# Kernel tuning notes

Measured on AMD Instinct MI355X. Metric: run time of the kernel, lower is better.

Reference implementation:

```python
import jax, jax.numpy as jnp
import numpy as np

N, D, E, C = 50000, 128, 500000, 2
K1, K2 = 3, 5


def spline_conv(x, src, dst, pseudo, W, root, bias, K, num_nodes):
    # degree-1 open B-spline basis over dim=1 pseudo coords in [0,1]
    v = pseudo[:, 0] * (K - 1)                      # [E]
    i0f = jnp.floor(v)
    frac = v - i0f                                   # [E]
    i0 = jnp.clip(i0f.astype(jnp.int32), 0, K - 1)
    i1 = jnp.clip(i0 + 1, 0, K - 1)
    xs = x[src]                                      # [E, D] gather
    # scatter basis-weighted neighbor feats into per-(node,kernel) buckets
    acc = jax.ops.segment_sum((1.0 - frac)[:, None] * xs, dst * K + i0,
                              num_segments=num_nodes * K)
    acc = acc + jax.ops.segment_sum(frac[:, None] * xs, dst * K + i1,
                                    num_segments=num_nodes * K)
    acc = acc.reshape(num_nodes, K, -1)              # [N, K, D]
    deg = jax.ops.segment_sum(jnp.ones_like(v), dst, num_segments=num_nodes)
    out = jnp.einsum('nkd,kdo->no', acc, W) / jnp.maximum(deg, 1.0)[:, None]
    return out + x @ root + bias                     # mean aggr + root + bias


def setup_inputs() -> dict:
    key = jax.random.key(0)
    ks = jax.random.split(key, 12)
    s = 1.0 / np.sqrt(D)
    return {
        'x': jax.random.normal(ks[0], (N, D), jnp.float32),
        'edge_index': jax.random.randint(ks[1], (2, E), 0, N, jnp.int64),
        'edge_attr': jax.random.uniform(ks[2], (E, 1), jnp.float32),
        'W1': jax.random.normal(ks[3], (K1, D, D), jnp.float32) * s,
        'root1': jax.random.normal(ks[4], (D, D), jnp.float32) * s,
        'b1': jnp.zeros((D,), jnp.float32),
        'W2': jax.random.normal(ks[5], (K2, D, D), jnp.float32) * s,
        'root2': jax.random.normal(ks[6], (D, D), jnp.float32) * s,
        'b2': jnp.zeros((D,), jnp.float32),
        'Wm': jax.random.normal(ks[7], (D, C), jnp.float32) * s,
        'bm': jnp.zeros((C,), jnp.float32),
    }


def reference(x, edge_index, edge_attr, W1, root1, b1, W2, root2, b2, Wm, bm):
    src, dst = edge_index[0], edge_index[1]
    h = jax.nn.elu(spline_conv(x, src, dst, edge_attr, W1, root1, b1, K1, N))
    # dropout is identity in eval mode
    h = jax.nn.elu(spline_conv(h, src, dst, edge_attr, W2, root2, b2, K2, N))
    return jax.nn.relu(h @ Wm + bm)                  # [N, C]
```

## Files before the change

kernel.cpp:

```cpp
#include <hip/hip_runtime.h>
#include <cmath>


typedef __attribute__((ext_vector_type(8))) short bf16x8;
typedef __attribute__((ext_vector_type(4))) float f32x4;

static inline int cdiv(int a, int b) { return (a + b - 1) / b; }

__device__ __forceinline__ float bf2f(unsigned short u) {
  unsigned v = ((unsigned)u) << 16;
  return __builtin_bit_cast(float, v);
}
__device__ __forceinline__ unsigned short f2bf(float f) {
  unsigned u = __builtin_bit_cast(unsigned, f);
  u += 0x7FFFu + ((u >> 16) & 1u);
  return (unsigned short)(u >> 16);
}
__device__ __forceinline__ float elu1(float v) {
  return v > 0.f ? v : (expf(v) - 1.f);
}

__global__ void hist_kernel(const int* __restrict__ ei, int E,
                            int* __restrict__ cnt) {
  int e = blockIdx.x * blockDim.x + threadIdx.x;
  if (e < E) atomicAdd(&cnt[ei[E + e]], 1);
}

__global__ void scan_partials_kernel(const int* __restrict__ cnt, int N,
                                     int* __restrict__ partials) {
  __shared__ int red[256];
  int base = blockIdx.x * 1024;
  int s = 0;
  for (int i = threadIdx.x; i < 1024; i += 256) {
    int idx = base + i;
    if (idx < N) s += cnt[idx];
  }
  red[threadIdx.x] = s;
  __syncthreads();
  for (int off = 128; off > 0; off >>= 1) {
    if (threadIdx.x < off) red[threadIdx.x] += red[threadIdx.x + off];
    __syncthreads();
  }
  if (threadIdx.x == 0) partials[blockIdx.x] = red[0];
}

__global__ void scan_pscan_kernel(const int* __restrict__ partials, int nb,
                                  int* __restrict__ pscan) {
  __shared__ int tmp[256];
  int t = threadIdx.x;
  int v = (t < nb) ? partials[t] : 0;
  tmp[t] = v;
  __syncthreads();
  for (int off = 1; off < 256; off <<= 1) {
    int u = (t >= off) ? tmp[t - off] : 0;
    __syncthreads();
    tmp[t] += u;
    __syncthreads();
  }
  pscan[t + 1] = tmp[t];
  if (t == 0) pscan[0] = 0;
}

__global__ void scan_apply_kernel(const int* __restrict__ cnt, int N,
                                  const int* __restrict__ pscan, int nb,
                                  int* __restrict__ rowptr, int* __restrict__ cursor) {
  __shared__ int tsum[256];
  int t = threadIdx.x;
  int base = blockIdx.x * 1024 + t * 4;
  int v0 = 0, v1 = 0, v2 = 0, v3 = 0;
  if (base + 0 < N) v0 = cnt[base + 0];
  if (base + 1 < N) v1 = cnt[base + 1];
  if (base + 2 < N) v2 = cnt[base + 2];
  if (base + 3 < N) v3 = cnt[base + 3];
  int s = v0 + v1 + v2 + v3;
  tsum[t] = s;
  __syncthreads();
  for (int off = 1; off < 256; off <<= 1) {
    int u = (t >= off) ? tsum[t - off] : 0;
    __syncthreads();
    tsum[t] += u;
    __syncthreads();
  }
  int excl = pscan[blockIdx.x] + tsum[t] - s;
  if (base + 0 < N) { rowptr[base + 0] = excl; cursor[base + 0] = excl; excl += v0; }
  if (base + 1 < N) { rowptr[base + 1] = excl; cursor[base + 1] = excl; excl += v1; }
  if (base + 2 < N) { rowptr[base + 2] = excl; cursor[base + 2] = excl; excl += v2; }
  if (base + 3 < N) { rowptr[base + 3] = excl; cursor[base + 3] = excl; excl += v3; }
  if (blockIdx.x == 0 && t == 0) rowptr[N] = pscan[nb];
}

__global__ void scatter_kernel(const int* __restrict__ ei,
                               const float* __restrict__ ea, int E,
                               int* __restrict__ cursor, int2* __restrict__ es) {
  int e = blockIdx.x * blockDim.x + threadIdx.x;
  if (e < E) {
    int dst = ei[E + e];
    int pos = atomicAdd(&cursor[dst], 1);
    es[pos] = make_int2(ei[e], __float_as_int(ea[e]));
  }
}

__global__ void cvt_x_kernel(const float* __restrict__ x,
                             unsigned short* __restrict__ xb, int n4) {
  for (int i = blockIdx.x * blockDim.x + threadIdx.x; i < n4;
       i += gridDim.x * blockDim.x) {
    float4 v = ((const float4*)x)[i];
    ushort4 o;
    o.x = f2bf(v.x); o.y = f2bf(v.y); o.z = f2bf(v.z); o.w = f2bf(v.w);
    ((ushort4*)xb)[i] = o;
  }
}

__global__ void build_btf_kernel(const float* __restrict__ W,
                                 const float* __restrict__ root,
                                 unsigned short* __restrict__ BtF, int KD, int KT) {
  int idx = blockIdx.x * blockDim.x + threadIdx.x;
  if (idx >= 128 * KT) return;
  int G = idx >> 9;
  int r = idx & 511;
  int lane = r >> 3;
  int j = r & 7;
  int ks = G >> 3;
  int ni = G & 7;
  int col = ni * 16 + (lane & 15);
  int k = ks * 32 + (lane >> 4) * 8 + j;
  float v = (k < KD) ? W[(size_t)k * 128 + col] : root[(size_t)(k - KD) * 128 + col];
  BtF[idx] = f2bf(v);
}

template <int K, int KT, bool FINAL>
__global__ __launch_bounds__(256, 4) void fused_layer(
    const unsigned short* __restrict__ Xc,
    const int* __restrict__ rowptr, const int2* __restrict__ es,
    const unsigned short* __restrict__ BtF,
    const float* __restrict__ bias,
    unsigned short* __restrict__ Hout,
    const float* __restrict__ Wm, const float* __restrict__ bm,
    float* __restrict__ FOut) {
  constexpr int LDK = KT + 8;
  constexpr int NKS = KT / 32;
  __shared__ unsigned short Asub[16][LDK];
  __shared__ float hred[4][16][2];

  const int w = threadIdx.x >> 6;
  const int lane = threadIdx.x & 63;
  const int lr = lane & 15;
  const int kg = lane >> 4;
  const int node0 = blockIdx.x * 16;

  for (int i = 0; i < 4; ++i) {
    const int r = w * 4 + i;
    const int node = node0 + r;
    float accx[K], accy[K];
#pragma unroll
    for (int k = 0; k < K; ++k) { accx[k] = 0.f; accy[k] = 0.f; }
    const int beg = rowptr[node], end = rowptr[node + 1];
    int e = beg;
    for (; e + 8 <= end; e += 8) {
      int2 sp[8];
#pragma unroll
      for (int t = 0; t < 8; ++t) sp[t] = es[e + t];
      ushort2 xv[8];
#pragma unroll
      for (int t = 0; t < 8; ++t)
        xv[t] = *(const ushort2*)(Xc + (size_t)sp[t].x * 128 + 2 * lane);
#pragma unroll
      for (int t = 0; t < 8; ++t) {
        float v = __int_as_float(sp[t].y) * (float)(K - 1);
        int i0 = min((int)v, K - 2);
        float fr = v - (float)i0;
        float w0 = 1.f - fr;
        float xx = bf2f(xv[t].x), xy = bf2f(xv[t].y);
        int i0u = __builtin_amdgcn_readfirstlane(i0);
#pragma unroll
        for (int k = 0; k < K - 1; ++k) {
          if (i0u == k) {
            accx[k] = fmaf(w0, xx, accx[k]);
            accy[k] = fmaf(w0, xy, accy[k]);
            accx[k + 1] = fmaf(fr, xx, accx[k + 1]);
            accy[k + 1] = fmaf(fr, xy, accy[k + 1]);
          }
        }
      }
    }
    for (; e < end; e += 4) {
      const int last = end - 1;
      int2 sp[4];
      bool okv[4];
#pragma unroll
      for (int t = 0; t < 4; ++t) {
        okv[t] = (e + t <= last);
        sp[t] = es[okv[t] ? (e + t) : last];
      }
      ushort2 xv[4];
#pragma unroll
      for (int t = 0; t < 4; ++t)
        xv[t] = *(const ushort2*)(Xc + (size_t)sp[t].x * 128 + 2 * lane);
#pragma unroll
      for (int t = 0; t < 4; ++t) {
        float v = __int_as_float(sp[t].y) * (float)(K - 1);
        int i0 = min((int)v, K - 2);
        float fr = v - (float)i0;
        float w0 = 1.f - fr;
        if (!okv[t]) { w0 = 0.f; fr = 0.f; }
        float xx = bf2f(xv[t].x), xy = bf2f(xv[t].y);
        int i0u = __builtin_amdgcn_readfirstlane(i0);
#pragma unroll
        for (int k = 0; k < K - 1; ++k) {
          if (i0u == k) {
            accx[k] = fmaf(w0, xx, accx[k]);
            accy[k] = fmaf(w0, xy, accy[k]);
            accx[k + 1] = fmaf(fr, xx, accx[k + 1]);
            accy[k + 1] = fmaf(fr, xy, accy[k + 1]);
          }
        }
      }
    }
    float deg = (float)(end - beg);
    float sc = 1.f / fmaxf(deg, 1.f);
#pragma unroll
    for (int k = 0; k < K; ++k) {
      ushort2 o;
      o.x = f2bf(accx[k] * sc);
      o.y = f2bf(accy[k] * sc);
      *(ushort2*)&Asub[r][k * 128 + 2 * lane] = o;
    }
    ushort2 own = *(const ushort2*)(Xc + (size_t)node * 128 + 2 * lane);
    *(ushort2*)&Asub[r][K * 128 + 2 * lane] = own;
  }
  __syncthreads();

  const int ni0 = w * 2;
  f32x4 acc[2];
  acc[0] = {0.f, 0.f, 0.f, 0.f};
  acc[1] = {0.f, 0.f, 0.f, 0.f};
#pragma unroll
  for (int ks = 0; ks < NKS; ++ks) {
    bf16x8 a = *(const bf16x8*)&Asub[lr][ks * 32 + kg * 8];
#pragma unroll
    for (int j = 0; j < 2; ++j) {
      bf16x8 b = *(const bf16x8*)(BtF + (size_t)(ks * 8 + ni0 + j) * 512 + lane * 8);
      acc[j] = __builtin_amdgcn_mfma_f32_16x16x32_bf16(a, b, acc[j], 0, 0, 0);
    }
  }

  float bv[2];
#pragma unroll
  for (int j = 0; j < 2; ++j) bv[j] = bias[(ni0 + j) * 16 + lr];

  if constexpr (!FINAL) {
#pragma unroll
    for (int r = 0; r < 4; ++r) {
      int row = kg * 4 + r;
      int node = node0 + row;
#pragma unroll
      for (int j = 0; j < 2; ++j) {
        float h = elu1(acc[j][r] + bv[j]);
        Hout[(size_t)node * 128 + (ni0 + j) * 16 + lr] = f2bf(h);
      }
    }
  } else {
    float wm0[2], wm1[2];
#pragma unroll
    for (int j = 0; j < 2; ++j) {
      float2 wv = *(const float2*)&Wm[((ni0 + j) * 16 + lr) * 2];
      wm0[j] = wv.x; wm1[j] = wv.y;
    }
#pragma unroll
    for (int r = 0; r < 4; ++r) {
      int row = kg * 4 + r;
      float t0 = 0.f, t1 = 0.f;
#pragma unroll
      for (int j = 0; j < 2; ++j) {
        float h = elu1(acc[j][r] + bv[j]);
        t0 = fmaf(h, wm0[j], t0);
        t1 = fmaf(h, wm1[j], t1);
      }
#pragma unroll
      for (int off = 8; off > 0; off >>= 1) {
        t0 += __shfl_down(t0, off);
        t1 += __shfl_down(t1, off);
      }
      if (lr == 0) {
        hred[w][row][0] = t0;
        hred[w][row][1] = t1;
      }
    }
    __syncthreads();
    if (threadIdx.x < 32) {
      int row = threadIdx.x >> 1;
      int c = threadIdx.x & 1;
      float s = hred[0][row][c] + hred[1][row][c] + hred[2][row][c] +
                hred[3][row][c] + bm[c];
      FOut[(size_t)(node0 + row) * 2 + c] = fmaxf(s, 0.f);
    }
  }
}

extern "C" void kernel_launch(void* const* d_in, const int* in_sizes, int n_in,
                              void* d_out, int out_size, void* d_ws, size_t ws_size,
                              hipStream_t stream) {
  const float* x = (const float*)d_in[0];
  const int* ei = (const int*)d_in[1];
  const float* ea = (const float*)d_in[2];
  const float* W1 = (const float*)d_in[3];
  const float* root1 = (const float*)d_in[4];
  const float* b1 = (const float*)d_in[5];
  const float* W2 = (const float*)d_in[6];
  const float* root2 = (const float*)d_in[7];
  const float* b2 = (const float*)d_in[8];
  const float* Wm = (const float*)d_in[9];
  const float* bm = (const float*)d_in[10];
  const int N = in_sizes[0] / 128;
  const int E = in_sizes[2];
  const int KT1 = 512, KT2 = 768;
  const int nb = cdiv(N, 1024);

  char* base = (char*)d_ws;
  size_t off = 0;
  auto alloc = [&](size_t bytes) -> void* {
    void* p = base + off;
    off += (bytes + 255) & ~(size_t)255;
    return p;
  };
  int* cnt = (int*)alloc((size_t)N * 4);
  int* rowptr = (int*)alloc((size_t)(N + 1) * 4);
  int* cursor = (int*)alloc((size_t)N * 4);
  int* partials = (int*)alloc(256 * 4);
  int* pscan = (int*)alloc(257 * 4);
  int2* es = (int2*)alloc((size_t)E * 8);
  unsigned short* xb = (unsigned short*)alloc((size_t)N * 128 * 2);
  unsigned short* h1 = (unsigned short*)alloc((size_t)N * 128 * 2);
  unsigned short* BtF1 = (unsigned short*)alloc((size_t)128 * KT1 * 2);
  unsigned short* BtF2 = (unsigned short*)alloc((size_t)128 * KT2 * 2);
  (void)ws_size; (void)n_in; (void)out_size;

  hipMemsetAsync(cnt, 0, (size_t)N * 4, stream);
  hist_kernel<<<cdiv(E, 256), 256, 0, stream>>>(ei, E, cnt);
  scan_partials_kernel<<<nb, 256, 0, stream>>>(cnt, N, partials);
  scan_pscan_kernel<<<1, 256, 0, stream>>>(partials, nb, pscan);
  scan_apply_kernel<<<nb, 256, 0, stream>>>(cnt, N, pscan, nb, rowptr, cursor);
  scatter_kernel<<<cdiv(E, 256), 256, 0, stream>>>(ei, ea, E, cursor, es);

  build_btf_kernel<<<cdiv(128 * KT1, 256), 256, 0, stream>>>(W1, root1, BtF1, 384, KT1);
  build_btf_kernel<<<cdiv(128 * KT2, 256), 256, 0, stream>>>(W2, root2, BtF2, 640, KT2);

  cvt_x_kernel<<<2048, 256, 0, stream>>>(x, xb, N * 32);

  const int nblk = N / 16;
  fused_layer<3, 512, false><<<nblk, 256, 0, stream>>>(
      xb, rowptr, es, BtF1, b1, h1, nullptr, nullptr, nullptr);
  fused_layer<5, 768, true><<<nblk, 256, 0, stream>>>(
      h1, rowptr, es, BtF2, b2, nullptr, Wm, bm, (float*)d_out);
}
```

Measured before the change: 189.3 us.

## Widen fused layer blocks to 32 nodes and gather edges in chunks of 16

```diff
diff --git a/kernel.cpp b/kernel.cpp
--- a/kernel.cpp
+++ b/kernel.cpp
@@ -128,94 +128,82 @@
   BtF[idx] = f2bf(v);
 }
 
+template <int K, bool MASK>
+__device__ __forceinline__ void agg_chunk16(
+    const unsigned short* __restrict__ Xc, const int2* __restrict__ es,
+    int e, int end, int lane, float (&accx)[K], float (&accy)[K]) {
+  const int last = end - 1;
+  int sx[16];
+  float pv[16];
+#pragma unroll
+  for (int t = 0; t < 16; ++t) {
+    int idx = MASK ? min(e + t, last) : (e + t);
+    int2 sp = es[idx];
+    sx[t] = sp.x;
+    pv[t] = __int_as_float(sp.y);
+  }
+  unsigned int dv[16];
+#pragma unroll
+  for (int t = 0; t < 16; ++t)
+    dv[t] = *(const unsigned int*)(Xc + (size_t)sx[t] * 128 + 2 * lane);
+#pragma unroll
+  for (int t = 0; t < 16; ++t) {
+    float v = pv[t] * (float)(K - 1);
+    int i0 = min((int)v, K - 2);
+    float fr = v - (float)i0;
+    float w0 = 1.f - fr;
+    if (MASK) {
+      bool ok = (e + t <= last);
+      fr = ok ? fr : 0.f;
+      w0 = ok ? w0 : 0.f;
+    }
+    float xx = __builtin_bit_cast(float, dv[t] << 16);
+    float xy = __builtin_bit_cast(float, dv[t] & 0xffff0000u);
+    int i0u = __builtin_amdgcn_readfirstlane(i0);
+#pragma unroll
+    for (int k = 0; k < K - 1; ++k) {
+      if (i0u == k) {
+        accx[k] = fmaf(w0, xx, accx[k]);
+        accy[k] = fmaf(w0, xy, accy[k]);
+        accx[k + 1] = fmaf(fr, xx, accx[k + 1]);
+        accy[k + 1] = fmaf(fr, xy, accy[k + 1]);
+      }
+    }
+  }
+}
+
 template <int K, int KT, bool FINAL>
-__global__ __launch_bounds__(256, 4) void fused_layer(
+__global__ __launch_bounds__(512, 6) void fused_layer(
     const unsigned short* __restrict__ Xc,
     const int* __restrict__ rowptr, const int2* __restrict__ es,
     const unsigned short* __restrict__ BtF,
     const float* __restrict__ bias,
     unsigned short* __restrict__ Hout,
     const float* __restrict__ Wm, const float* __restrict__ bm,
-    float* __restrict__ FOut) {
+    float* __restrict__ FOut, int N) {
   constexpr int LDK = KT + 8;
   constexpr int NKS = KT / 32;
-  __shared__ unsigned short Asub[16][LDK];
-  __shared__ float hred[4][16][2];
+  __shared__ unsigned short Asub[32][LDK];
+  __shared__ float hred[8][32][2];
 
   const int w = threadIdx.x >> 6;
   const int lane = threadIdx.x & 63;
   const int lr = lane & 15;
   const int kg = lane >> 4;
-  const int node0 = blockIdx.x * 16;
+  const int node0 = blockIdx.x * 32;
 
   for (int i = 0; i < 4; ++i) {
     const int r = w * 4 + i;
-    const int node = node0 + r;
+    const int node = min(node0 + r, N - 1);
     float accx[K], accy[K];
 #pragma unroll
     for (int k = 0; k < K; ++k) { accx[k] = 0.f; accy[k] = 0.f; }
     const int beg = rowptr[node], end = rowptr[node + 1];
     int e = beg;
-    for (; e + 8 <= end; e += 8) {
-      int2 sp[8];
-#pragma unroll
-      for (int t = 0; t < 8; ++t) sp[t] = es[e + t];
-      ushort2 xv[8];
-#pragma unroll
-      for (int t = 0; t < 8; ++t)
-        xv[t] = *(const ushort2*)(Xc + (size_t)sp[t].x * 128 + 2 * lane);
-#pragma unroll
-      for (int t = 0; t < 8; ++t) {
-        float v = __int_as_float(sp[t].y) * (float)(K - 1);
-        int i0 = min((int)v, K - 2);
-        float fr = v - (float)i0;
-        float w0 = 1.f - fr;
-        float xx = bf2f(xv[t].x), xy = bf2f(xv[t].y);
-        int i0u = __builtin_amdgcn_readfirstlane(i0);
-#pragma unroll
-        for (int k = 0; k < K - 1; ++k) {
-          if (i0u == k) {
-            accx[k] = fmaf(w0, xx, accx[k]);
-            accy[k] = fmaf(w0, xy, accy[k]);
-            accx[k + 1] = fmaf(fr, xx, accx[k + 1]);
-            accy[k + 1] = fmaf(fr, xy, accy[k + 1]);
-          }
-        }
-      }
-    }
-    for (; e < end; e += 4) {
-      const int last = end - 1;
-      int2 sp[4];
-      bool okv[4];
-#pragma unroll
-      for (int t = 0; t < 4; ++t) {
-        okv[t] = (e + t <= last);
-        sp[t] = es[okv[t] ? (e + t) : last];
-      }
-      ushort2 xv[4];
-#pragma unroll
-      for (int t = 0; t < 4; ++t)
-        xv[t] = *(const ushort2*)(Xc + (size_t)sp[t].x * 128 + 2 * lane);
-#pragma unroll
-      for (int t = 0; t < 4; ++t) {
-        float v = __int_as_float(sp[t].y) * (float)(K - 1);
-        int i0 = min((int)v, K - 2);
-        float fr = v - (float)i0;
-        float w0 = 1.f - fr;
-        if (!okv[t]) { w0 = 0.f; fr = 0.f; }
-        float xx = bf2f(xv[t].x), xy = bf2f(xv[t].y);
-        int i0u = __builtin_amdgcn_readfirstlane(i0);
-#pragma unroll
-        for (int k = 0; k < K - 1; ++k) {
-          if (i0u == k) {
-            accx[k] = fmaf(w0, xx, accx[k]);
-            accy[k] = fmaf(w0, xy, accy[k]);
-            accx[k + 1] = fmaf(fr, xx, accx[k + 1]);
-            accy[k + 1] = fmaf(fr, xy, accy[k + 1]);
-          }
-        }
-      }
-    }
+    for (; e + 16 <= end; e += 16)
+      agg_chunk16<K, false>(Xc, es, e, end, lane, accx, accy);
+    if (e < end)
+      agg_chunk16<K, true>(Xc, es, e, end, lane, accx, accy);
     float deg = (float)(end - beg);
     float sc = 1.f / fmaxf(deg, 1.f);
 #pragma unroll
@@ -230,69 +218,67 @@
   }
   __syncthreads();
 
-  const int ni0 = w * 2;
-  f32x4 acc[2];
-  acc[0] = {0.f, 0.f, 0.f, 0.f};
-  acc[1] = {0.f, 0.f, 0.f, 0.f};
+  const int ni = w;
+  f32x4 acc0 = {0.f, 0.f, 0.f, 0.f};
+  f32x4 acc1 = {0.f, 0.f, 0.f, 0.f};
+  __builtin_amdgcn_s_setprio(1);
 #pragma unroll
   for (int ks = 0; ks < NKS; ++ks) {
-    bf16x8 a = *(const bf16x8*)&Asub[lr][ks * 32 + kg * 8];
-#pragma unroll
-    for (int j = 0; j < 2; ++j) {
-      bf16x8 b = *(const bf16x8*)(BtF + (size_t)(ks * 8 + ni0 + j) * 512 + lane * 8);
-      acc[j] = __builtin_amdgcn_mfma_f32_16x16x32_bf16(a, b, acc[j], 0, 0, 0);
-    }
-  }
-
-  float bv[2];
-#pragma unroll
-  for (int j = 0; j < 2; ++j) bv[j] = bias[(ni0 + j) * 16 + lr];
+    bf16x8 b = *(const bf16x8*)(BtF + (size_t)(ks * 8 + ni) * 512 + lane * 8);
+    bf16x8 a0 = *(const bf16x8*)&Asub[lr][ks * 32 + kg * 8];
+    bf16x8 a1 = *(const bf16x8*)&Asub[16 + lr][ks * 32 + kg * 8];
+    acc0 = __builtin_amdgcn_mfma_f32_16x16x32_bf16(a0, b, acc0, 0, 0, 0);
+    acc1 = __builtin_amdgcn_mfma_f32_16x16x32_bf16(a1, b, acc1, 0, 0, 0);
+  }
+  __builtin_amdgcn_s_setprio(0);
+
+  const float bv = bias[ni * 16 + lr];
 
   if constexpr (!FINAL) {
 #pragma unroll
-    for (int r = 0; r < 4; ++r) {
-      int row = kg * 4 + r;
-      int node = node0 + row;
-#pragma unroll
-      for (int j = 0; j < 2; ++j) {
-        float h = elu1(acc[j][r] + bv[j]);
-        Hout[(size_t)node * 128 + (ni0 + j) * 16 + lr] = f2bf(h);
+    for (int mf = 0; mf < 2; ++mf) {
+      f32x4 a = mf ? acc1 : acc0;
+#pragma unroll
+      for (int r = 0; r < 4; ++r) {
+        int node = node0 + mf * 16 + kg * 4 + r;
+        if (node < N) {
+          float h = elu1(a[r] + bv);
+          Hout[(size_t)node * 128 + ni * 16 + lr] = f2bf(h);
+        }
       }
     }
   } else {
-    float wm0[2], wm1[2];
-#pragma unroll
-    for (int j = 0; j < 2; ++j) {
-      float2 wv = *(const float2*)&Wm[((ni0 + j) * 16 + lr) * 2];
-      wm0[j] = wv.x; wm1[j] = wv.y;
-    }
-#pragma unroll
-    for (int r = 0; r < 4; ++r) {
-      int row = kg * 4 + r;
-      float t0 = 0.f, t1 = 0.f;
-#pragma unroll
-      for (int j = 0; j < 2; ++j) {
-        float h = elu1(acc[j][r] + bv[j]);
-        t0 = fmaf(h, wm0[j], t0);
-        t1 = fmaf(h, wm1[j], t1);
+    float2 wv = *(const float2*)&Wm[(ni * 16 + lr) * 2];
+#pragma unroll
+    for (int mf = 0; mf < 2; ++mf) {
+      f32x4 a = mf ? acc1 : acc0;
+#pragma unroll
+      for (int r = 0; r < 4; ++r) {
+        float h = elu1(a[r] + bv);
+        float t0 = h * wv.x;
+        float t1 = h * wv.y;
+#pragma unroll
+        for (int off = 8; off > 0; off >>= 1) {
+          t0 += __shfl_down(t0, off);
+          t1 += __shfl_down(t1, off);
+        }
+        if (lr == 0) {
+          hred[w][mf * 16 + kg * 4 + r][0] = t0;
+          hred[w][mf * 16 + kg * 4 + r][1] = t1;
+        }
       }
-#pragma unroll
-      for (int off = 8; off > 0; off >>= 1) {
-        t0 += __shfl_down(t0, off);
-        t1 += __shfl_down(t1, off);
-      }
-      if (lr == 0) {
-        hred[w][row][0] = t0;
-        hred[w][row][1] = t1;
-      }
-    }
-    __syncthreads();
-    if (threadIdx.x < 32) {
+    }
+    __syncthreads();
+    if (threadIdx.x < 64) {
       int row = threadIdx.x >> 1;
       int c = threadIdx.x & 1;
-      float s = hred[0][row][c] + hred[1][row][c] + hred[2][row][c] +
-                hred[3][row][c] + bm[c];
-      FOut[(size_t)(node0 + row) * 2 + c] = fmaxf(s, 0.f);
+      int node = node0 + row;
+      if (node < N) {
+        float s = bm[c];
+#pragma unroll
+        for (int ww = 0; ww < 8; ++ww) s += hred[ww][row][c];
+        FOut[(size_t)node * 2 + c] = fmaxf(s, 0.f);
+      }
     }
   }
 }
@@ -347,9 +333,9 @@
 
   cvt_x_kernel<<<2048, 256, 0, stream>>>(x, xb, N * 32);
 
-  const int nblk = N / 16;
-  fused_layer<3, 512, false><<<nblk, 256, 0, stream>>>(
-      xb, rowptr, es, BtF1, b1, h1, nullptr, nullptr, nullptr);
-  fused_layer<5, 768, true><<<nblk, 256, 0, stream>>>(
-      h1, rowptr, es, BtF2, b2, nullptr, Wm, bm, (float*)d_out);
-}
+  const int nblk = cdiv(N, 32);
+  fused_layer<3, 512, false><<<nblk, 512, 0, stream>>>(
+      xb, rowptr, es, BtF1, b1, h1, nullptr, nullptr, nullptr, N);
+  fused_layer<5, 768, true><<<nblk, 512, 0, stream>>>(
+      h1, rowptr, es, BtF2, b2, nullptr, Wm, bm, (float*)d_out, N);
+}
```

After: 362.1 us. 91.3% more time.

## Process four nodes per wavefront with 16-byte row gathers and branchless spline weights

Applied to the files above, without the earlier changes.

```diff
diff --git a/kernel.cpp b/kernel.cpp
--- a/kernel.cpp
+++ b/kernel.cpp
@@ -148,99 +148,79 @@
   const int kg = lane >> 4;
   const int node0 = blockIdx.x * 16;
 
-  for (int i = 0; i < 4; ++i) {
-    const int r = w * 4 + i;
-    const int node = node0 + r;
-    float accx[K], accy[K];
-#pragma unroll
-    for (int k = 0; k < K; ++k) { accx[k] = 0.f; accy[k] = 0.f; }
-    const int beg = rowptr[node], end = rowptr[node + 1];
-    int e = beg;
-    for (; e + 8 <= end; e += 8) {
-      int2 sp[8];
-#pragma unroll
-      for (int t = 0; t < 8; ++t) sp[t] = es[e + t];
-      ushort2 xv[8];
-#pragma unroll
-      for (int t = 0; t < 8; ++t)
-        xv[t] = *(const ushort2*)(Xc + (size_t)sp[t].x * 128 + 2 * lane);
-#pragma unroll
-      for (int t = 0; t < 8; ++t) {
-        float v = __int_as_float(sp[t].y) * (float)(K - 1);
-        int i0 = min((int)v, K - 2);
-        float fr = v - (float)i0;
-        float w0 = 1.f - fr;
-        float xx = bf2f(xv[t].x), xy = bf2f(xv[t].y);
-        int i0u = __builtin_amdgcn_readfirstlane(i0);
-#pragma unroll
-        for (int k = 0; k < K - 1; ++k) {
-          if (i0u == k) {
-            accx[k] = fmaf(w0, xx, accx[k]);
-            accy[k] = fmaf(w0, xy, accy[k]);
-            accx[k + 1] = fmaf(fr, xx, accx[k + 1]);
-            accy[k + 1] = fmaf(fr, xy, accy[k + 1]);
-          }
-        }
-      }
-    }
-    for (; e < end; e += 4) {
-      const int last = end - 1;
-      int2 sp[4];
-      bool okv[4];
-#pragma unroll
-      for (int t = 0; t < 4; ++t) {
-        okv[t] = (e + t <= last);
-        sp[t] = es[okv[t] ? (e + t) : last];
-      }
-      ushort2 xv[4];
-#pragma unroll
-      for (int t = 0; t < 4; ++t)
-        xv[t] = *(const ushort2*)(Xc + (size_t)sp[t].x * 128 + 2 * lane);
-#pragma unroll
-      for (int t = 0; t < 4; ++t) {
-        float v = __int_as_float(sp[t].y) * (float)(K - 1);
-        int i0 = min((int)v, K - 2);
-        float fr = v - (float)i0;
-        float w0 = 1.f - fr;
-        if (!okv[t]) { w0 = 0.f; fr = 0.f; }
-        float xx = bf2f(xv[t].x), xy = bf2f(xv[t].y);
-        int i0u = __builtin_amdgcn_readfirstlane(i0);
-#pragma unroll
-        for (int k = 0; k < K - 1; ++k) {
-          if (i0u == k) {
-            accx[k] = fmaf(w0, xx, accx[k]);
-            accy[k] = fmaf(w0, xy, accy[k]);
-            accx[k + 1] = fmaf(fr, xx, accx[k + 1]);
-            accy[k + 1] = fmaf(fr, xy, accy[k + 1]);
-          }
-        }
-      }
-    }
-    float deg = (float)(end - beg);
-    float sc = 1.f / fmaxf(deg, 1.f);
-#pragma unroll
-    for (int k = 0; k < K; ++k) {
-      ushort2 o;
-      o.x = f2bf(accx[k] * sc);
-      o.y = f2bf(accy[k] * sc);
-      *(ushort2*)&Asub[r][k * 128 + 2 * lane] = o;
-    }
-    ushort2 own = *(const ushort2*)(Xc + (size_t)node * 128 + 2 * lane);
-    *(ushort2*)&Asub[r][K * 128 + 2 * lane] = own;
-  }
+  const int g = lane >> 4;
+  const int d16 = lane & 15;
+  const int r = w * 4 + g;
+  const int node = node0 + r;
+  const int beg = rowptr[node];
+  const int end = rowptr[node + 1];
+  const int deg = end - beg;
+
+  float acc[K][8];
+#pragma unroll
+  for (int k = 0; k < K; ++k)
+#pragma unroll
+    for (int j = 0; j < 8; ++j) acc[k][j] = 0.f;
+
+  const int mx = max(max(__shfl(deg, 0), __shfl(deg, 16)),
+                     max(__shfl(deg, 32), __shfl(deg, 48)));
+  const int lastc = max(end - 1, 0);
+
+  for (int s0 = 0; s0 < mx; s0 += 4) {
+    int2 sp[4];
+#pragma unroll
+    for (int t = 0; t < 4; ++t) sp[t] = es[min(beg + s0 + t, lastc)];
+    uint4 rv[4];
+#pragma unroll
+    for (int t = 0; t < 4; ++t)
+      rv[t] = *(const uint4*)(Xc + (size_t)sp[t].x * 128 + d16 * 8);
+#pragma unroll
+    for (int t = 0; t < 4; ++t) {
+      const bool ok = (s0 + t) < deg;
+      const float v = ok ? __int_as_float(sp[t].y) * (float)(K - 1) : -2.f;
+      float x[8];
+      x[0] = __builtin_bit_cast(float, rv[t].x << 16);
+      x[1] = __builtin_bit_cast(float, rv[t].x & 0xffff0000u);
+      x[2] = __builtin_bit_cast(float, rv[t].y << 16);
+      x[3] = __builtin_bit_cast(float, rv[t].y & 0xffff0000u);
+      x[4] = __builtin_bit_cast(float, rv[t].z << 16);
+      x[5] = __builtin_bit_cast(float, rv[t].z & 0xffff0000u);
+      x[6] = __builtin_bit_cast(float, rv[t].w << 16);
+      x[7] = __builtin_bit_cast(float, rv[t].w & 0xffff0000u);
+#pragma unroll
+      for (int k = 0; k < K; ++k) {
+        const float wk = fmaxf(1.f - fabsf(v - (float)k), 0.f);
+#pragma unroll
+        for (int j = 0; j < 8; ++j) acc[k][j] = fmaf(wk, x[j], acc[k][j]);
+      }
+    }
+  }
+
+  const float sc = 1.f / fmaxf((float)deg, 1.f);
+#pragma unroll
+  for (int k = 0; k < K; ++k) {
+    uint4 ov;
+    ov.x = (unsigned)f2bf(acc[k][0] * sc) | ((unsigned)f2bf(acc[k][1] * sc) << 16);
+    ov.y = (unsigned)f2bf(acc[k][2] * sc) | ((unsigned)f2bf(acc[k][3] * sc) << 16);
+    ov.z = (unsigned)f2bf(acc[k][4] * sc) | ((unsigned)f2bf(acc[k][5] * sc) << 16);
+    ov.w = (unsigned)f2bf(acc[k][6] * sc) | ((unsigned)f2bf(acc[k][7] * sc) << 16);
+    *(uint4*)&Asub[r][k * 128 + d16 * 8] = ov;
+  }
+  uint4 ownv = *(const uint4*)(Xc + (size_t)node * 128 + d16 * 8);
+  *(uint4*)&Asub[r][K * 128 + d16 * 8] = ownv;
   __syncthreads();
 
   const int ni0 = w * 2;
-  f32x4 acc[2];
-  acc[0] = {0.f, 0.f, 0.f, 0.f};
-  acc[1] = {0.f, 0.f, 0.f, 0.f};
+  f32x4 acc2[2];
+  acc2[0] = {0.f, 0.f, 0.f, 0.f};
+  acc2[1] = {0.f, 0.f, 0.f, 0.f};
 #pragma unroll
   for (int ks = 0; ks < NKS; ++ks) {
     bf16x8 a = *(const bf16x8*)&Asub[lr][ks * 32 + kg * 8];
 #pragma unroll
     for (int j = 0; j < 2; ++j) {
       bf16x8 b = *(const bf16x8*)(BtF + (size_t)(ks * 8 + ni0 + j) * 512 + lane * 8);
-      acc[j] = __builtin_amdgcn_mfma_f32_16x16x32_bf16(a, b, acc[j], 0, 0, 0);
+      acc2[j] = __builtin_amdgcn_mfma_f32_16x16x32_bf16(a, b, acc2[j], 0, 0, 0);
     }
   }
 
@@ -250,13 +230,13 @@
 
   if constexpr (!FINAL) {
 #pragma unroll
-    for (int r = 0; r < 4; ++r) {
-      int row = kg * 4 + r;
-      int node = node0 + row;
+    for (int rr = 0; rr < 4; ++rr) {
+      int row = kg * 4 + rr;
+      int onode = node0 + row;
 #pragma unroll
       for (int j = 0; j < 2; ++j) {
-        float h = elu1(acc[j][r] + bv[j]);
-        Hout[(size_t)node * 128 + (ni0 + j) * 16 + lr] = f2bf(h);
+        float h = elu1(acc2[j][rr] + bv[j]);
+        Hout[(size_t)onode * 128 + (ni0 + j) * 16 + lr] = f2bf(h);
       }
     }
   } else {
@@ -267,12 +247,12 @@
       wm0[j] = wv.x; wm1[j] = wv.y;
     }
 #pragma unroll
-    for (int r = 0; r < 4; ++r) {
-      int row = kg * 4 + r;
+    for (int rr = 0; rr < 4; ++rr) {
+      int row = kg * 4 + rr;
       float t0 = 0.f, t1 = 0.f;
 #pragma unroll
       for (int j = 0; j < 2; ++j) {
-        float h = elu1(acc[j][r] + bv[j]);
+        float h = elu1(acc2[j][rr] + bv[j]);
         t0 = fmaf(h, wm0[j], t0);
         t1 = fmaf(h, wm1[j], t1);
       }
```

Result: faster. 163.9 us, median of 2 (-13.4%).
